# Kernel optimization log

Measured on AMD Instinct MI355X. Metric: run time of the kernel, lower is better.

The kernel has to match this reference:

```python
import jax, jax.numpy as jnp
import numpy as np

B, D_IN, H, D_OUT = 4096, 4096, 2048, 1000
LN_EPS = 1e-5


def setup_inputs() -> dict:
    key = jax.random.key(0)
    ks = jax.random.split(key, 8)
    s_in = 1.0 / np.sqrt(H)  # torch RNN init: U(-1/sqrt(H), 1/sqrt(H))
    inp = {
        "x": jax.random.normal(ks[0], (B, D_IN), dtype=jnp.float32),
        "W_ih0": jax.random.uniform(ks[1], (H, D_IN), jnp.float32, -s_in, s_in),
        "b_ih0": jax.random.uniform(ks[2], (H,), jnp.float32, -s_in, s_in),
        "b_hh0": jax.random.uniform(ks[3], (H,), jnp.float32, -s_in, s_in),
        "W_ih1": jax.random.uniform(ks[4], (H, H), jnp.float32, -s_in, s_in),
        "b_ih1": jax.random.uniform(ks[5], (H,), jnp.float32, -s_in, s_in),
        "b_hh1": jax.random.uniform(ks[6], (H,), jnp.float32, -s_in, s_in),
        "ln_g": jnp.ones((2 * H,), jnp.float32),
        "ln_b": jnp.zeros((2 * H,), jnp.float32),
        "fc_W": jax.random.uniform(ks[7], (D_OUT, 2 * H), jnp.float32, -1.0 / np.sqrt(2 * H), 1.0 / np.sqrt(2 * H)),
        "fc_b": jnp.zeros((D_OUT,), jnp.float32),
    }
    return inp


def reference(x, W_ih0, b_ih0, b_hh0, W_ih1, b_ih1, b_hh1, ln_g, ln_b, fc_W, fc_b):
    # seq_len == 1, h0 == 0 -> W_hh terms vanish; only biases remain.
    h1 = jnp.tanh(x @ W_ih0.T + b_ih0 + b_hh0)          # [B, H]
    h2 = jnp.tanh(h1 @ W_ih1.T + b_ih1 + b_hh1)         # [B, H]
    # last_hidden == mean_pooled (single step) -> concat duplicates h2
    combined = jnp.concatenate([h2, h2], axis=1)        # [B, 2H]
    mu = combined.mean(axis=-1, keepdims=True)
    var = combined.var(axis=-1, keepdims=True)
    normed = (combined - mu) * jax.lax.rsqrt(var + LN_EPS) * ln_g + ln_b
    # dropout is identity in eval mode
    return normed @ fc_W.T + fc_b                        # [B, D_OUT]
```

## Files before the change

### kernel.cpp

```cpp
#include <hip/hip_runtime.h>
#include <hip/hip_bf16.h>

typedef __attribute__((ext_vector_type(8))) unsigned short ushort8;
typedef __attribute__((ext_vector_type(8))) __bf16 bf16x8;
typedef __attribute__((ext_vector_type(4))) float f32x4;
typedef __attribute__((ext_vector_type(4))) float floatx4;

__device__ __forceinline__ unsigned short f2bf(float f) {
    unsigned u = __builtin_bit_cast(unsigned, f);
    u += 0x7fffu + ((u >> 16) & 1u);
    return (unsigned short)(u >> 16);
}
__device__ __forceinline__ float bf2f(unsigned short h) {
    unsigned u = ((unsigned)h) << 16;
    return __builtin_bit_cast(float, u);
}

__device__ __forceinline__ void gload_lds16(const void* g, void* l) {
    __builtin_amdgcn_global_load_lds(
        (const __attribute__((address_space(1))) void*)g,
        (__attribute__((address_space(3))) void*)l,
        16, 0, 0);
}

#define BAR()   asm volatile("s_barrier" ::: "memory")
#define VMW4()  asm volatile("s_waitcnt vmcnt(4)" ::: "memory")
#define VMW2()  asm volatile("s_waitcnt vmcnt(2)" ::: "memory")
#define VMW0()  asm volatile("s_waitcnt vmcnt(0)" ::: "memory")

__global__ __launch_bounds__(256) void cvt_f2bf(const float* __restrict__ in,
                                                unsigned short* __restrict__ out,
                                                int n8) {
    int i = blockIdx.x * 256 + threadIdx.x;
    if (i >= n8) return;
    floatx4 a = ((const floatx4*)in)[2 * i];
    floatx4 b = ((const floatx4*)in)[2 * i + 1];
    ushort8 o;
#pragma unroll
    for (int j = 0; j < 4; ++j) { o[j] = f2bf(a[j]); o[4 + j] = f2bf(b[j]); }
    ((ushort8*)out)[i] = o;
}

__global__ __launch_bounds__(256) void weff_kernel(const float* __restrict__ fcW,
                                                   const float* __restrict__ lng,
                                                   const float* __restrict__ lnb,
                                                   const float* __restrict__ fcb,
                                                   unsigned short* __restrict__ weff,
                                                   float* __restrict__ cc,
                                                   float* __restrict__ wsum) {
    int o = blockIdx.x;
    int tid = threadIdx.x;
    if (o >= 1000) {
        ushort8 z = {0, 0, 0, 0, 0, 0, 0, 0};
        ((ushort8*)(weff + (size_t)o * 2048))[tid] = z;
        if (tid == 0) { cc[o] = 0.f; wsum[o] = 0.f; }
        return;
    }
    const float* wrow = fcW + (size_t)o * 4096;
    int j0 = tid * 8;
    floatx4 wa  = *(const floatx4*)(wrow + j0);
    floatx4 wb  = *(const floatx4*)(wrow + j0 + 4);
    floatx4 wa2 = *(const floatx4*)(wrow + 2048 + j0);
    floatx4 wb2 = *(const floatx4*)(wrow + 2048 + j0 + 4);
    floatx4 ga  = *(const floatx4*)(lng + j0);
    floatx4 gb  = *(const floatx4*)(lng + j0 + 4);
    floatx4 ga2 = *(const floatx4*)(lng + 2048 + j0);
    floatx4 gb2 = *(const floatx4*)(lng + 2048 + j0 + 4);
    floatx4 ba  = *(const floatx4*)(lnb + j0);
    floatx4 bb  = *(const floatx4*)(lnb + j0 + 4);
    floatx4 ba2 = *(const floatx4*)(lnb + 2048 + j0);
    floatx4 bb2 = *(const floatx4*)(lnb + 2048 + j0 + 4);
    ushort8 o8;
    float acc = 0.f, ws = 0.f;
#pragma unroll
    for (int j = 0; j < 4; ++j) {
        o8[j] = f2bf(ga[j] * wa[j] + ga2[j] * wa2[j]);
        acc += ba[j] * wa[j] + ba2[j] * wa2[j];
        ws  += bf2f(o8[j]);
        o8[4 + j] = f2bf(gb[j] * wb[j] + gb2[j] * wb2[j]);
        acc += bb[j] * wb[j] + bb2[j] * wb2[j];
        ws  += bf2f(o8[4 + j]);
    }
    ((ushort8*)(weff + (size_t)o * 2048))[tid] = o8;
#pragma unroll
    for (int d = 32; d; d >>= 1) { acc += __shfl_down(acc, d); ws += __shfl_down(ws, d); }
    __shared__ float red[4], redw[4];
    if ((tid & 63) == 0) { red[tid >> 6] = acc; redw[tid >> 6] = ws; }
    __syncthreads();
    if (tid == 0) {
        cc[o] = fcb[o] + red[0] + red[1] + red[2] + red[3];
        wsum[o] = redw[0] + redw[1] + redw[2] + redw[3];
    }
}

__global__ __launch_bounds__(256) void ln_stats(const unsigned short* __restrict__ h2,
                                                float2* __restrict__ mur) {
    int row = blockIdx.x, tid = threadIdx.x;
    ushort8 v = ((const ushort8*)(h2 + (size_t)row * 2048))[tid];
    float s = 0.f, s2 = 0.f;
#pragma unroll
    for (int j = 0; j < 8; ++j) { float f = bf2f(v[j]); s += f; s2 += f * f; }
#pragma unroll
    for (int d = 32; d; d >>= 1) { s += __shfl_down(s, d); s2 += __shfl_down(s2, d); }
    __shared__ float rs_[4], rs2_[4];
    if ((tid & 63) == 0) { rs_[tid >> 6] = s; rs2_[tid >> 6] = s2; }
    __syncthreads();
    if (tid == 0) {
        float S = rs_[0] + rs_[1] + rs_[2] + rs_[3];
        float S2 = rs2_[0] + rs2_[1] + rs2_[2] + rs2_[3];
        float mu = S * (1.f / 2048.f);
        float var = S2 * (1.f / 2048.f) - mu * mu;
        mur[row] = make_float2(mu, rsqrtf(var + 1e-5f));
    }
}

__global__ __launch_bounds__(256) void reduce_tanh(const unsigned short* __restrict__ P0,
                                                   const unsigned short* __restrict__ P1,
                                                   const float* __restrict__ b0,
                                                   const float* __restrict__ b1,
                                                   unsigned short* __restrict__ out) {
    int i = blockIdx.x * 256 + threadIdx.x;
    ushort8 p0 = ((const ushort8*)P0)[i];
    ushort8 p1 = ((const ushort8*)P1)[i];
    int c0 = (i * 8) & 2047;
    floatx4 ba = *(const floatx4*)(b0 + c0), bb = *(const floatx4*)(b0 + c0 + 4);
    floatx4 ca = *(const floatx4*)(b1 + c0), cb = *(const floatx4*)(b1 + c0 + 4);
    ushort8 o;
#pragma unroll
    for (int j = 0; j < 4; ++j) {
        o[j]     = f2bf(tanhf(bf2f(p0[j])     + bf2f(p1[j])     + ba[j] + ca[j]));
        o[4 + j] = f2bf(tanhf(bf2f(p0[4 + j]) + bf2f(p1[4 + j]) + bb[j] + cb[j]));
    }
    ((ushort8*)out)[i] = o;
}

__global__ __launch_bounds__(512, 2) void gemm256(const unsigned short* __restrict__ A,
                                                  const unsigned short* __restrict__ B,
                                                  int Ks, int KP, int N,
                                                  unsigned short* __restrict__ Pa,
                                                  unsigned short* __restrict__ Pb) {
    extern __shared__ char smem[];
    const int tid = threadIdx.x;
    const int lane = tid & 63, wid = tid >> 6;
    const int wm = wid >> 2, wn = wid & 3;
    const int fr = lane & 15, g = lane >> 4;
    const int kp = blockIdx.z;

    const int gx = gridDim.x;
    const int nwg = gx * gridDim.y;
    const int fid = blockIdx.y * gx + blockIdx.x;
    const int cpx = nwg >> 3;
    const int sw = (fid & 7) * cpx + (fid >> 3);
    const int bx = sw % gx, by = sw / gx;
    const int row0 = by * 256, col0 = bx * 256;
    const int kbase = kp * KP;

    char* bufA0 = smem;
    char* bufB0 = smem + 32768;

    const int rl = tid >> 3;
    const int sl = tid & 7;
    const int scol = ((sl ^ (rl & 7)) * 8);

    auto stageA = [&](int kt, int half, char* bufb) {
        const size_t koff = (size_t)(kbase + kt * 64 + scol);
#pragma unroll
        for (int gg = 0; gg < 2; ++gg) {
            int r = half * 128 + gg * 64;
            gload_lds16(A + (size_t)(row0 + r + rl) * Ks + koff,
                        bufb + r * 128 + wid * 1024);
        }
    };
    auto stageB = [&](int kt, int half, char* bufb) {
        const size_t koff = (size_t)(kbase + kt * 64 + scol);
#pragma unroll
        for (int gg = 0; gg < 2; ++gg) {
            int r = half * 128 + gg * 64;
            gload_lds16(B + (size_t)(col0 + r + rl) * Ks + koff,
                        bufb + 32768 + r * 128 + wid * 1024);
        }
    };

    const int xorv = (fr & 7) << 4;
    auto readA = [&](bf16x8 (&fa)[4][2], const char* bufb, int hi) {
#pragma unroll
        for (int m = 0; m < 4; ++m) {
            int row = hi * 128 + wm * 64 + m * 16 + fr;
#pragma unroll
            for (int kh = 0; kh < 2; ++kh)
                fa[m][kh] = __builtin_bit_cast(bf16x8, *(const ushort8*)(
                    bufb + row * 128 + ((kh * 64 + g * 16) ^ xorv)));
        }
    };
    auto readB = [&](bf16x8 (&fb)[2][2], const char* bufb, int bh) {
#pragma unroll
        for (int n = 0; n < 2; ++n) {
            int row = bh * 128 + wn * 32 + n * 16 + fr;
#pragma unroll
            for (int kh = 0; kh < 2; ++kh)
                fb[n][kh] = __builtin_bit_cast(bf16x8, *(const ushort8*)(
                    bufb + 32768 + row * 128 + ((kh * 64 + g * 16) ^ xorv)));
        }
    };

    f32x4 acc[8][4];
#pragma unroll
    for (int i = 0; i < 8; ++i)
#pragma unroll
        for (int j = 0; j < 4; ++j) acc[i][j] = f32x4{0.f, 0.f, 0.f, 0.f};

    bf16x8 aF[4][2], b0[2][2], b1[2][2];

    stageA(0, 0, smem); stageB(0, 0, smem); stageB(0, 1, smem); stageA(0, 1, smem);

    const int NT = KP >> 6;
    for (int t = 0; t < NT; ++t) {
        char* rb = smem + (t & 1) * 65536;
        char* wb = smem + ((t + 1) & 1) * 65536;
        const bool st = (t + 1) < NT;

        VMW4();
        BAR();
        if (st) stageA(t + 1, 0, wb);
        readA(aF, rb, 0);
        readB(b0, rb, 0);
        __builtin_amdgcn_s_setprio(1);
#pragma unroll
        for (int m = 0; m < 4; ++m)
#pragma unroll
            for (int n = 0; n < 2; ++n)
#pragma unroll
                for (int kh = 0; kh < 2; ++kh)
                    acc[m][n] = __builtin_amdgcn_mfma_f32_16x16x32_bf16(aF[m][kh], b0[n][kh], acc[m][n], 0, 0, 0);
        __builtin_amdgcn_s_setprio(0);
        BAR();

        if (st) { VMW4(); } else { VMW2(); }
        BAR();
        if (st) stageB(t + 1, 0, wb);
        readB(b1, rb, 1);
        __builtin_amdgcn_s_setprio(1);
#pragma unroll
        for (int m = 0; m < 4; ++m)
#pragma unroll
            for (int n = 0; n < 2; ++n)
#pragma unroll
                for (int kh = 0; kh < 2; ++kh)
                    acc[m][2 + n] = __builtin_amdgcn_mfma_f32_16x16x32_bf16(aF[m][kh], b1[n][kh], acc[m][2 + n], 0, 0, 0);
        __builtin_amdgcn_s_setprio(0);
        BAR();

        if (st) { VMW4(); } else { VMW0(); }
        BAR();
        if (st) stageB(t + 1, 1, wb);
        readA(aF, rb, 1);
        __builtin_amdgcn_s_setprio(1);
#pragma unroll
        for (int m = 0; m < 4; ++m)
#pragma unroll
            for (int n = 0; n < 2; ++n)
#pragma unroll
                for (int kh = 0; kh < 2; ++kh)
                    acc[4 + m][2 + n] = __builtin_amdgcn_mfma_f32_16x16x32_bf16(aF[m][kh], b1[n][kh], acc[4 + m][2 + n], 0, 0, 0);
        __builtin_amdgcn_s_setprio(0);
        BAR();

        if (st) stageA(t + 1, 1, wb);
        __builtin_amdgcn_s_setprio(1);
#pragma unroll
        for (int m = 0; m < 4; ++m)
#pragma unroll
            for (int n = 0; n < 2; ++n)
#pragma unroll
                for (int kh = 0; kh < 2; ++kh)
                    acc[4 + m][n] = __builtin_amdgcn_mfma_f32_16x16x32_bf16(aF[m][kh], b0[n][kh], acc[4 + m][n], 0, 0, 0);
        __builtin_amdgcn_s_setprio(0);
        BAR();
    }

    unsigned short* P = kp ? Pb : Pa;
#pragma unroll
    for (int i = 0; i < 8; ++i) {
        int hi = i >> 2, m = i & 3;
        int rbase = row0 + hi * 128 + wm * 64 + m * 16 + g * 4;
#pragma unroll
        for (int j = 0; j < 4; ++j) {
            int bh = j >> 1, n = j & 1;
            int col = col0 + bh * 128 + wn * 32 + n * 16 + fr;
#pragma unroll
            for (int r = 0; r < 4; ++r)
                P[(size_t)(rbase + r) * N + col] = f2bf(acc[i][j][r]);
        }
    }
}

template <int EPI, int NJ>
__global__ __launch_bounds__(512, 2) void gemm_rp(const unsigned short* __restrict__ A,
                                                  const unsigned short* __restrict__ B,
                                                  int M, int N, int K,
                                                  const float* __restrict__ bias0,
                                                  const float* __restrict__ bias1,
                                                  void* __restrict__ Cout, int ncols,
                                                  const float2* __restrict__ mur,
                                                  const float* __restrict__ wsum) {
    extern __shared__ char smem[];
    constexpr int BUFSZ = 16384 + NJ * 8192;
    const int tid = threadIdx.x;
    const int lane = tid & 63, wid = tid >> 6;
    const int wm = wid >> 2, wn = wid & 3;
    const int fr = lane & 15, g = lane >> 4;

    const int nwg = gridDim.x * gridDim.y;
    const int fid = blockIdx.y * gridDim.x + blockIdx.x;
    const int cpx = nwg >> 3;
    const int sw = (fid & 7) * cpx + (fid >> 3);
    const int bx = sw % gridDim.x, by = sw / gridDim.x;
    const int row0 = by * 128, col0 = bx * (64 * NJ);

    const int tg = tid >> 3;
    const int tcE = ((tid & 7) ^ (tg & 7)) * 8;

    auto stage = [&](int kt, char* buf) {
#pragma unroll
        for (int r = 0; r < 2; ++r)
            gload_lds16(A + (size_t)(row0 + r * 64 + tg) * K + kt * 64 + tcE,
                        buf + r * 8192 + wid * 1024);
#pragma unroll
        for (int rr = 0; rr < NJ; ++rr)
            gload_lds16(B + (size_t)(col0 + rr * 64 + tg) * K + kt * 64 + tcE,
                        buf + 16384 + rr * 8192 + wid * 1024);
    };

    const int xorv = (fr & 7) << 4;
    auto readFrags = [&](bf16x8 (&fa)[4][2], bf16x8 (&fb)[NJ][2], const char* buf) {
#pragma unroll
        for (int m = 0; m < 4; ++m)
#pragma unroll
            for (int kh = 0; kh < 2; ++kh)
                fa[m][kh] = __builtin_bit_cast(bf16x8, *(const ushort8*)(
                    buf + (wm * 64 + m * 16 + fr) * 128 + ((kh * 64 + g * 16) ^ xorv)));
#pragma unroll
        for (int n = 0; n < NJ; ++n)
#pragma unroll
            for (int kh = 0; kh < 2; ++kh)
                fb[n][kh] = __builtin_bit_cast(bf16x8, *(const ushort8*)(
                    buf + 16384 + (wn * (16 * NJ) + n * 16 + fr) * 128 + ((kh * 64 + g * 16) ^ xorv)));
    };

    f32x4 acc[4][NJ];
#pragma unroll
    for (int i = 0; i < 4; ++i)
#pragma unroll
        for (int j = 0; j < NJ; ++j) acc[i][j] = f32x4{0.f, 0.f, 0.f, 0.f};

    auto domfma = [&](bf16x8 (&fa)[4][2], bf16x8 (&fb)[NJ][2]) {
        __builtin_amdgcn_s_setprio(1);
#pragma unroll
        for (int m = 0; m < 4; ++m)
#pragma unroll
            for (int n = 0; n < NJ; ++n)
#pragma unroll
                for (int kh = 0; kh < 2; ++kh)
                    acc[m][n] = __builtin_amdgcn_mfma_f32_16x16x32_bf16(fa[m][kh], fb[n][kh], acc[m][n], 0, 0, 0);
        __builtin_amdgcn_s_setprio(0);
    };

    bf16x8 aX[4][2], bX[NJ][2], aY[4][2], bY[NJ][2];

    stage(0, smem); stage(1, smem + BUFSZ);
    if constexpr (NJ == 4) { asm volatile("s_waitcnt vmcnt(6)" ::: "memory"); }
    else                   { asm volatile("s_waitcnt vmcnt(4)" ::: "memory"); }
    BAR();
    readFrags(aX, bX, smem);

    const int NT = K >> 6;
    for (int t = 0; t < NT; t += 2) {
        if (t + 2 < NT) {
            stage(t + 2, smem + ((t + 2) % 3) * BUFSZ);
            if constexpr (NJ == 4) { asm volatile("s_waitcnt vmcnt(6)" ::: "memory"); }
            else                   { asm volatile("s_waitcnt vmcnt(4)" ::: "memory"); }
        } else {
            VMW0();
        }
        BAR();
        readFrags(aY, bY, smem + ((t + 1) % 3) * BUFSZ);
        domfma(aX, bX);

        if (t + 2 < NT) {
            if (t + 3 < NT) {
                stage(t + 3, smem + ((t + 3) % 3) * BUFSZ);
                if constexpr (NJ == 4) { asm volatile("s_waitcnt vmcnt(6)" ::: "memory"); }
                else                   { asm volatile("s_waitcnt vmcnt(4)" ::: "memory"); }
            } else {
                VMW0();
            }
            BAR();
            readFrags(aX, bX, smem + ((t + 2) % 3) * BUFSZ);
        }
        domfma(aY, bY);
    }

#pragma unroll
    for (int i = 0; i < 4; ++i) {
        int rbase = row0 + wm * 64 + i * 16 + g * 4;
        if (EPI == 0) {
#pragma unroll
            for (int j = 0; j < NJ; ++j) {
                int col = col0 + wn * (16 * NJ) + j * 16 + fr;
                float bsum = bias0[col] + bias1[col];
                unsigned short* O = (unsigned short*)Cout;
#pragma unroll
                for (int r = 0; r < 4; ++r)
                    O[(size_t)(rbase + r) * N + col] = f2bf(tanhf(acc[i][j][r] + bsum));
            }
        } else {
            float2 mr[4];
#pragma unroll
            for (int r = 0; r < 4; ++r) mr[r] = mur[rbase + r];
#pragma unroll
            for (int j = 0; j < NJ; ++j) {
                int col = col0 + wn * (16 * NJ) + j * 16 + fr;
                if (col < ncols) {
                    float ws = wsum[col];
                    float ccv = bias0[col];
                    float* O = (float*)Cout;
#pragma unroll
                    for (int r = 0; r < 4; ++r)
                        O[(size_t)(rbase + r) * ncols + col] =
                            mr[r].y * (acc[i][j][r] - mr[r].x * ws) + ccv;
                }
            }
        }
    }
}

extern "C" void kernel_launch(void* const* d_in, const int* in_sizes, int n_in,
                              void* d_out, int out_size, void* d_ws, size_t ws_size,
                              hipStream_t stream) {
    const float* x   = (const float*)d_in[0];
    const float* W0  = (const float*)d_in[1];
    const float* bi0 = (const float*)d_in[2];
    const float* bh0 = (const float*)d_in[3];
    const float* W1  = (const float*)d_in[4];
    const float* bi1 = (const float*)d_in[5];
    const float* bh1 = (const float*)d_in[6];
    const float* lng = (const float*)d_in[7];
    const float* lnb = (const float*)d_in[8];
    const float* fcW = (const float*)d_in[9];
    const float* fcb = (const float*)d_in[10];
    float* out = (float*)d_out;

    char* w = (char*)d_ws;
    unsigned short* xb   = (unsigned short*)(w);
    unsigned short* w0b  = (unsigned short*)(w + 33554432ull);
    unsigned short* w1b  = (unsigned short*)(w + 50331648ull);
    unsigned short* h1   = (unsigned short*)(w + 58720256ull);
    unsigned short* h2   = (unsigned short*)(w + 75497472ull);
    unsigned short* weff = (unsigned short*)(w + 92274688ull);
    float* cc            = (float*)(w + 96468992ull);
    float* wsum          = (float*)(w + 96473088ull);
    float2* mur          = (float2*)(w + 96477184ull);
    unsigned short* P1a  = h2;
    unsigned short* P1b  = (unsigned short*)(w + 96509952ull);
    unsigned short* P2a  = xb;
    unsigned short* P2b  = (unsigned short*)(w + 16777216ull);

    const int SHM256 = 131072;
    const int SHM1 = 3 * (16384 + 2 * 8192);
    (void)hipFuncSetAttribute((const void*)gemm256,
                              hipFuncAttributeMaxDynamicSharedMemorySize, SHM256);
    (void)hipFuncSetAttribute((const void*)gemm_rp<1, 2>,
                              hipFuncAttributeMaxDynamicSharedMemorySize, SHM1);

    cvt_f2bf<<<8192, 256, 0, stream>>>(x,  xb,  2097152);
    cvt_f2bf<<<4096, 256, 0, stream>>>(W0, w0b, 1048576);
    cvt_f2bf<<<2048, 256, 0, stream>>>(W1, w1b, 524288);
    weff_kernel<<<1024, 256, 0, stream>>>(fcW, lng, lnb, fcb, weff, cc, wsum);

    gemm256<<<dim3(8, 16, 2), 512, SHM256, stream>>>(xb, w0b, 4096, 2048, 2048, P1a, P1b);
    reduce_tanh<<<4096, 256, 0, stream>>>(P1a, P1b, bi0, bh0, h1);

    gemm256<<<dim3(8, 16, 2), 512, SHM256, stream>>>(h1, w1b, 2048, 1024, 2048, P2a, P2b);
    reduce_tanh<<<4096, 256, 0, stream>>>(P2a, P2b, bi1, bh1, h2);

    ln_stats<<<4096, 256, 0, stream>>>(h2, mur);
    gemm_rp<1, 2><<<dim3(8, 32), 512, SHM1, stream>>>(h2, weff, 4096, 1024, 2048,
                                                      cc, nullptr, out, 1000, mur, wsum);
}
```

Measured before the change: 183.9 us.

## Restructure 256x256 GEMM pipeline with contiguous warp tiles and lgkm-based sync

Rewrites the two split-K bf16 GEMMs' main loop. Each warp now owns a contiguous 128x64 output tile instead of interleaved halves. Next-tile staging is issued as whole A and B blocks after the LDS fragment reads, and the per-quarter vmcnt waits become lgkmcnt waits plus sched_barriers, with a single vmcnt(0) drain per k-tile. The aim is to overlap LDS reads, global-to-LDS loads and MFMA more cleanly. The trade-off is less fine-grained wait control on global loads.

```diff
diff --git a/kernel.cpp b/kernel.cpp
--- a/kernel.cpp
+++ b/kernel.cpp
@@ -24,9 +24,10 @@
 }
 
 #define BAR()   asm volatile("s_barrier" ::: "memory")
-#define VMW4()  asm volatile("s_waitcnt vmcnt(4)" ::: "memory")
-#define VMW2()  asm volatile("s_waitcnt vmcnt(2)" ::: "memory")
 #define VMW0()  asm volatile("s_waitcnt vmcnt(0)" ::: "memory")
+#define LGK0()  asm volatile("s_waitcnt lgkmcnt(0)" ::: "memory")
+#define LGK8()  asm volatile("s_waitcnt lgkmcnt(8)" ::: "memory")
+#define SCHB0() __builtin_amdgcn_sched_barrier(0)
 
 __global__ __launch_bounds__(256) void cvt_f2bf(const float* __restrict__ in,
                                                 unsigned short* __restrict__ out,
@@ -134,11 +135,11 @@
     ((ushort8*)out)[i] = o;
 }
 
-__global__ __launch_bounds__(512, 2) void gemm256(const unsigned short* __restrict__ A,
-                                                  const unsigned short* __restrict__ B,
-                                                  int Ks, int KP, int N,
-                                                  unsigned short* __restrict__ Pa,
-                                                  unsigned short* __restrict__ Pb) {
+__global__ __launch_bounds__(512, 2) void gemm256p(const unsigned short* __restrict__ A,
+                                                   const unsigned short* __restrict__ B,
+                                                   int Ks, int KP, int N,
+                                                   unsigned short* __restrict__ Pa,
+                                                   unsigned short* __restrict__ Pb) {
     extern __shared__ char smem[];
     const int tid = threadIdx.x;
     const int lane = tid & 63, wid = tid >> 6;
@@ -155,53 +156,26 @@
     const int row0 = by * 256, col0 = bx * 256;
     const int kbase = kp * KP;
 
-    char* bufA0 = smem;
-    char* bufB0 = smem + 32768;
-
-    const int rl = tid >> 3;
-    const int sl = tid & 7;
-    const int scol = ((sl ^ (rl & 7)) * 8);
-
-    auto stageA = [&](int kt, int half, char* bufb) {
-        const size_t koff = (size_t)(kbase + kt * 64 + scol);
-#pragma unroll
-        for (int gg = 0; gg < 2; ++gg) {
-            int r = half * 128 + gg * 64;
-            gload_lds16(A + (size_t)(row0 + r + rl) * Ks + koff,
-                        bufb + r * 128 + wid * 1024);
-        }
+    const int srow = tid >> 3;
+    const int scolE = ((tid & 7) ^ ((tid >> 3) & 7)) * 8;
+    auto stageA = [&](int kt, char* buf) {
+        const size_t koff = (size_t)(kbase + kt * 64 + scolE);
+#pragma unroll
+        for (int gg = 0; gg < 4; ++gg)
+            gload_lds16(A + (size_t)(row0 + gg * 64 + srow) * Ks + koff,
+                        buf + gg * 8192 + wid * 1024);
     };
-    auto stageB = [&](int kt, int half, char* bufb) {
-        const size_t koff = (size_t)(kbase + kt * 64 + scol);
-#pragma unroll
-        for (int gg = 0; gg < 2; ++gg) {
-            int r = half * 128 + gg * 64;
-            gload_lds16(B + (size_t)(col0 + r + rl) * Ks + koff,
-                        bufb + 32768 + r * 128 + wid * 1024);
-        }
+    auto stageB = [&](int kt, char* buf) {
+        const size_t koff = (size_t)(kbase + kt * 64 + scolE);
+#pragma unroll
+        for (int gg = 0; gg < 4; ++gg)
+            gload_lds16(B + (size_t)(col0 + gg * 64 + srow) * Ks + koff,
+                        buf + 32768 + gg * 8192 + wid * 1024);
     };
 
     const int xorv = (fr & 7) << 4;
-    auto readA = [&](bf16x8 (&fa)[4][2], const char* bufb, int hi) {
-#pragma unroll
-        for (int m = 0; m < 4; ++m) {
-            int row = hi * 128 + wm * 64 + m * 16 + fr;
-#pragma unroll
-            for (int kh = 0; kh < 2; ++kh)
-                fa[m][kh] = __builtin_bit_cast(bf16x8, *(const ushort8*)(
-                    bufb + row * 128 + ((kh * 64 + g * 16) ^ xorv)));
-        }
-    };
-    auto readB = [&](bf16x8 (&fb)[2][2], const char* bufb, int bh) {
-#pragma unroll
-        for (int n = 0; n < 2; ++n) {
-            int row = bh * 128 + wn * 32 + n * 16 + fr;
-#pragma unroll
-            for (int kh = 0; kh < 2; ++kh)
-                fb[n][kh] = __builtin_bit_cast(bf16x8, *(const ushort8*)(
-                    bufb + 32768 + row * 128 + ((kh * 64 + g * 16) ^ xorv)));
-        }
-    };
+
+#define LDF(p) __builtin_bit_cast(bf16x8, *(const ushort8*)(p))
 
     f32x4 acc[8][4];
 #pragma unroll
@@ -209,9 +183,11 @@
 #pragma unroll
         for (int j = 0; j < 4; ++j) acc[i][j] = f32x4{0.f, 0.f, 0.f, 0.f};
 
-    bf16x8 aF[4][2], b0[2][2], b1[2][2];
-
-    stageA(0, 0, smem); stageB(0, 0, smem); stageB(0, 1, smem); stageA(0, 1, smem);
+    bf16x8 aF[4][2], b01[2][2], b23[2][2];
+
+    stageA(0, smem); stageB(0, smem);
+    VMW0();
+    BAR();
 
     const int NT = KP >> 6;
     for (int t = 0; t < NT; ++t) {
@@ -219,11 +195,20 @@
         char* wb = smem + ((t + 1) & 1) * 65536;
         const bool st = (t + 1) < NT;
 
-        VMW4();
-        BAR();
-        if (st) stageA(t + 1, 0, wb);
-        readA(aF, rb, 0);
-        readB(b0, rb, 0);
+#pragma unroll
+        for (int m = 0; m < 4; ++m)
+#pragma unroll
+            for (int kh = 0; kh < 2; ++kh)
+                aF[m][kh] = LDF(rb + (wm * 128 + m * 16 + fr) * 128 + ((kh * 64 + g * 16) ^ xorv));
+#pragma unroll
+        for (int n = 0; n < 2; ++n)
+#pragma unroll
+            for (int kh = 0; kh < 2; ++kh)
+                b01[n][kh] = LDF(rb + 32768 + (wn * 64 + n * 16 + fr) * 128 + ((kh * 64 + g * 16) ^ xorv));
+        if (st) stageA(t + 1, wb);
+        LGK8();
+        BAR();
+        LGK0(); SCHB0();
         __builtin_amdgcn_s_setprio(1);
 #pragma unroll
         for (int m = 0; m < 4; ++m)
@@ -231,14 +216,18 @@
             for (int n = 0; n < 2; ++n)
 #pragma unroll
                 for (int kh = 0; kh < 2; ++kh)
-                    acc[m][n] = __builtin_amdgcn_mfma_f32_16x16x32_bf16(aF[m][kh], b0[n][kh], acc[m][n], 0, 0, 0);
+                    acc[m][n] = __builtin_amdgcn_mfma_f32_16x16x32_bf16(aF[m][kh], b01[n][kh], acc[m][n], 0, 0, 0);
         __builtin_amdgcn_s_setprio(0);
         BAR();
 
-        if (st) { VMW4(); } else { VMW2(); }
-        BAR();
-        if (st) stageB(t + 1, 0, wb);
-        readB(b1, rb, 1);
+#pragma unroll
+        for (int n = 0; n < 2; ++n)
+#pragma unroll
+            for (int kh = 0; kh < 2; ++kh)
+                b23[n][kh] = LDF(rb + 32768 + (wn * 64 + (2 + n) * 16 + fr) * 128 + ((kh * 64 + g * 16) ^ xorv));
+        if (st) stageB(t + 1, wb);
+        BAR();
+        LGK0(); SCHB0();
         __builtin_amdgcn_s_setprio(1);
 #pragma unroll
         for (int m = 0; m < 4; ++m)
@@ -246,14 +235,17 @@
             for (int n = 0; n < 2; ++n)
 #pragma unroll
                 for (int kh = 0; kh < 2; ++kh)
-                    acc[m][2 + n] = __builtin_amdgcn_mfma_f32_16x16x32_bf16(aF[m][kh], b1[n][kh], acc[m][2 + n], 0, 0, 0);
+                    acc[m][2 + n] = __builtin_amdgcn_mfma_f32_16x16x32_bf16(aF[m][kh], b23[n][kh], acc[m][2 + n], 0, 0, 0);
         __builtin_amdgcn_s_setprio(0);
         BAR();
 
-        if (st) { VMW4(); } else { VMW0(); }
-        BAR();
-        if (st) stageB(t + 1, 1, wb);
-        readA(aF, rb, 1);
+#pragma unroll
+        for (int m = 0; m < 4; ++m)
+#pragma unroll
+            for (int kh = 0; kh < 2; ++kh)
+                aF[m][kh] = LDF(rb + (wm * 128 + (4 + m) * 16 + fr) * 128 + ((kh * 64 + g * 16) ^ xorv));
+        BAR();
+        LGK0(); SCHB0();
         __builtin_amdgcn_s_setprio(1);
 #pragma unroll
         for (int m = 0; m < 4; ++m)
@@ -261,11 +253,12 @@
             for (int n = 0; n < 2; ++n)
 #pragma unroll
                 for (int kh = 0; kh < 2; ++kh)
-                    acc[4 + m][2 + n] = __builtin_amdgcn_mfma_f32_16x16x32_bf16(aF[m][kh], b1[n][kh], acc[4 + m][2 + n], 0, 0, 0);
+                    acc[4 + m][2 + n] = __builtin_amdgcn_mfma_f32_16x16x32_bf16(aF[m][kh], b23[n][kh], acc[4 + m][2 + n], 0, 0, 0);
         __builtin_amdgcn_s_setprio(0);
         BAR();
 
-        if (st) stageA(t + 1, 1, wb);
+        VMW0();
+        BAR();
         __builtin_amdgcn_s_setprio(1);
 #pragma unroll
         for (int m = 0; m < 4; ++m)
@@ -273,25 +266,24 @@
             for (int n = 0; n < 2; ++n)
 #pragma unroll
                 for (int kh = 0; kh < 2; ++kh)
-                    acc[4 + m][n] = __builtin_amdgcn_mfma_f32_16x16x32_bf16(aF[m][kh], b0[n][kh], acc[4 + m][n], 0, 0, 0);
+                    acc[4 + m][n] = __builtin_amdgcn_mfma_f32_16x16x32_bf16(aF[m][kh], b01[n][kh], acc[4 + m][n], 0, 0, 0);
         __builtin_amdgcn_s_setprio(0);
         BAR();
     }
 
     unsigned short* P = kp ? Pb : Pa;
 #pragma unroll
-    for (int i = 0; i < 8; ++i) {
-        int hi = i >> 2, m = i & 3;
-        int rbase = row0 + hi * 128 + wm * 64 + m * 16 + g * 4;
-#pragma unroll
-        for (int j = 0; j < 4; ++j) {
-            int bh = j >> 1, n = j & 1;
-            int col = col0 + bh * 128 + wn * 32 + n * 16 + fr;
+    for (int m = 0; m < 8; ++m) {
+        int rbase = row0 + wm * 128 + m * 16 + g * 4;
+#pragma unroll
+        for (int n = 0; n < 4; ++n) {
+            int col = col0 + wn * 64 + n * 16 + fr;
 #pragma unroll
             for (int r = 0; r < 4; ++r)
-                P[(size_t)(rbase + r) * N + col] = f2bf(acc[i][j][r]);
+                P[(size_t)(rbase + r) * N + col] = f2bf(acc[m][n][r]);
         }
     }
+#undef LDF
 }
 
 template <int EPI, int NJ>
@@ -467,7 +459,7 @@
 
     const int SHM256 = 131072;
     const int SHM1 = 3 * (16384 + 2 * 8192);
-    (void)hipFuncSetAttribute((const void*)gemm256,
+    (void)hipFuncSetAttribute((const void*)gemm256p,
                               hipFuncAttributeMaxDynamicSharedMemorySize, SHM256);
     (void)hipFuncSetAttribute((const void*)gemm_rp<1, 2>,
                               hipFuncAttributeMaxDynamicSharedMemorySize, SHM1);
@@ -477,10 +469,10 @@
     cvt_f2bf<<<2048, 256, 0, stream>>>(W1, w1b, 524288);
     weff_kernel<<<1024, 256, 0, stream>>>(fcW, lng, lnb, fcb, weff, cc, wsum);
 
-    gemm256<<<dim3(8, 16, 2), 512, SHM256, stream>>>(xb, w0b, 4096, 2048, 2048, P1a, P1b);
+    gemm256p<<<dim3(8, 16, 2), 512, SHM256, stream>>>(xb, w0b, 4096, 2048, 2048, P1a, P1b);
     reduce_tanh<<<4096, 256, 0, stream>>>(P1a, P1b, bi0, bh0, h1);
 
-    gemm256<<<dim3(8, 16, 2), 512, SHM256, stream>>>(h1, w1b, 2048, 1024, 2048, P2a, P2b);
+    gemm256p<<<dim3(8, 16, 2), 512, SHM256, stream>>>(h1, w1b, 2048, 1024, 2048, P2a, P2b);
     reduce_tanh<<<4096, 256, 0, stream>>>(P2a, P2b, bi1, bh1, h2);
 
     ln_stats<<<4096, 256, 0, stream>>>(h2, mur);
```

Result: no change. 180.6 us (-1.8%).
